# Kernel optimization log

Hardware: AMD Instinct MI355X
Metric: run time of the kernel (lower is better)

Reference implementation:

```python
import jax, jax.numpy as jnp
import numpy as np

L = 2
GRID_RES = 0.01
ATOL = 0.01
RTOL = 1e-5  # torch.isclose default rtol


def _grad_matrices(filtration, bar, sample_pts):
    # filtration: [S,2] simplex (x,y) filtration values
    # bar:        [P,R] bar length per sample point, per rank
    # sample_pts: [P,2] center points
    S = filtration.shape[0]
    P, R = bar.shape
    shift = jnp.arange(-L, L + 1, dtype=filtration.dtype)          # [5]
    fx = filtration[:, 0]
    fy = filtration[:, 1]
    ptx = sample_pts[:, 0]
    pty = sample_pts[:, 1]
    scale = bar + GRID_RES                                          # [P,R]
    line_x = shift[None, None, :] * scale[:, :, None] + ptx[:, None, None]  # [P,R,5]
    line_y = shift[None, None, :] * scale[:, :, None] + pty[:, None, None]  # [P,R,5]
    last_x = line_x[:, :, -1]                                       # [P,R]
    last_y = line_y[:, :, -1]                                       # [P,R]
    # torch.isclose(a, b, atol): |a-b| <= atol + rtol*|b|
    tol_x = ATOL + RTOL * jnp.abs(fx)                               # [S]
    tol_y = ATOL + RTOL * jnp.abs(fy)
    close_x = jnp.any(jnp.abs(line_x[:, :, None, :] - fx[None, None, :, None])
                      <= tol_x[None, None, :, None], axis=-1)       # [P,R,S]
    close_y = jnp.any(jnp.abs(line_y[:, :, None, :] - fy[None, None, :, None])
                      <= tol_y[None, None, :, None], axis=-1)       # [P,R,S]
    fsum = fx + fy                                                  # [S]
    psum = (ptx + pty)[:, None, None]                               # [P,1,1]
    below = fsum[None, None, :] < psum                              # [P,1,S]
    above = fsum[None, None, :] > psum
    cond_x = close_x & (fy[None, None, :] <= last_y[:, :, None])    # [P,R,S]
    cond_y = close_y & (fx[None, None, :] <= last_x[:, :, None])
    lower_x = cond_x & below
    upper_x = cond_x & above
    lower_y = cond_y & below
    upper_y = cond_y & above
    gx = jnp.where(upper_x, 1.0, jnp.where(lower_x, -1.0, 0.0))     # [P,R,S]
    gy = jnp.where(upper_y, 1.0, jnp.where(lower_y, -1.0, 0.0))
    # interleave x/y per simplex: columns (2s, 2s+1)
    gm = jnp.stack([gx, gy], axis=-1).reshape(P, R, 2 * S).transpose(1, 0, 2)  # [R,P,2S]
    any_s = lambda m: jnp.any(m, axis=2)                            # [P,R]
    cx = jnp.where(any_s(upper_x), -1.0, jnp.where(any_s(lower_x), 1.0, 0.0))
    cy = jnp.where(any_s(upper_y), -1.0, jnp.where(any_s(lower_y), 1.0, 0.0))
    gc = jnp.stack([cx, cy], axis=-1).transpose(1, 0, 2)            # [R,P,2]
    return gm, gc


def setup_inputs() -> dict:
    key = jax.random.key(0)
    k1, k2, k3, k4 = jax.random.split(key, 4)
    S, P, R = 2000, 2500, 5
    filtration = jax.random.uniform(k1, (S, 2), dtype=jnp.float32)
    bars_h0 = jax.random.uniform(k2, (P, R), dtype=jnp.float32)
    bars_h1 = jax.random.uniform(k3, (P, R), dtype=jnp.float32)
    sample_pts = jax.random.uniform(k4, (P, 2), dtype=jnp.float32)
    return {"filtration": filtration, "bars_h0": bars_h0,
            "bars_h1": bars_h1, "sample_pts": sample_pts}


def reference(filtration, bars_h0, bars_h1, sample_pts):
    # moveSimplices.forward: passes bars through and builds the sparse
    # per-point gradient matrices (the dominant compute) for H0 and H1.
    gm0, gc0 = _grad_matrices(filtration, bars_h0, sample_pts)
    gm1, gc1 = _grad_matrices(filtration, bars_h1, sample_pts)
    out = jnp.stack([bars_h0, bars_h1])  # forward returns (bars[0], bars[1])
    return out, gm0, gc0, gm1, gc1
```

## Files before the change

### kernel.cpp

```cpp
#include <hip/hip_runtime.h>

#define S 2000
#define P 2500
#define R 5
#define HALF (S / 2)
#define NIT 16

typedef float floatx4 __attribute__((ext_vector_type(4)));

__global__ __launch_bounds__(256) void grad_kernel(
    const float* __restrict__ filtration,
    const float* __restrict__ bars0,
    const float* __restrict__ bars1,
    const float* __restrict__ sample_pts,
    float* __restrict__ out,
    float* __restrict__ gm0, float* __restrict__ gc0,
    float* __restrict__ gm1, float* __restrict__ gc1)
{
    __shared__ floatx4 sf[HALF];

    int tid = threadIdx.x;
    const floatx4* filt4 = (const floatx4*)filtration;
#pragma unroll
    for (int i = 0; i < NIT / 4; ++i) {
        int idx = tid + 256 * i;
        if (idx < HALF) sf[idx] = filt4[idx];
    }

    int job = blockIdx.x * 4 + (tid >> 6);
    int lane = tid & 63;
    int h = job / (R * P);
    int rem = job - h * (R * P);
    int r = rem / P;
    int p = rem - r * P;

    const float* bars = h ? bars1 : bars0;
    float* gm = h ? gm1 : gm0;
    float* gc = h ? gc1 : gc0;

    float bar = bars[p * R + r];
    float scale = bar + 0.01f;
    float ptx = sample_pts[2 * p];
    float pty = sample_pts[2 * p + 1];
    float psum = ptx + pty;

    float lxk[5], lyk[5];
#pragma unroll
    for (int k = 0; k < 5; ++k) {
        float ks = (float)(k - 2) * scale;
        lxk[k] = ks + ptx;
        lyk[k] = ks + pty;
    }
    float lastx = lxk[4];
    float lasty = lyk[4];

    if (lane == 0) out[(size_t)h * (P * R) + p * R + r] = bar;

    float* gmrow = gm + ((size_t)rem) * (size_t)(2 * S);

    bool aUx = false, aLx = false, aUy = false, aLy = false;

    __syncthreads();

#pragma unroll
    for (int it = 0; it < NIT; ++it) {
        int j = lane + 64 * it;
        if (it < NIT - 1 || j < HALF) {
            floatx4 f = sf[j];
            floatx4 o;
            {
                float fx = f.x, fy = f.y;
                float tolx = __fadd_rn(0.01f, __fmul_rn(1e-5f, __builtin_fabsf(fx)));
                float toly = __fadd_rn(0.01f, __fmul_rn(1e-5f, __builtin_fabsf(fy)));
                float mx = fminf(fminf(fminf(__builtin_fabsf(lxk[0] - fx),
                                             __builtin_fabsf(lxk[1] - fx)),
                                       fminf(__builtin_fabsf(lxk[2] - fx),
                                             __builtin_fabsf(lxk[3] - fx))),
                                 __builtin_fabsf(lxk[4] - fx));
                float my = fminf(fminf(fminf(__builtin_fabsf(lyk[0] - fy),
                                             __builtin_fabsf(lyk[1] - fy)),
                                       fminf(__builtin_fabsf(lyk[2] - fy),
                                             __builtin_fabsf(lyk[3] - fy))),
                                 __builtin_fabsf(lyk[4] - fy));
                bool cx = (mx <= tolx) && (fy <= lasty);
                bool cy = (my <= toly) && (fx <= lastx);
                float fsum = fx + fy;
                bool ab = fsum > psum, be = fsum < psum;
                float sgn = ab ? 1.0f : (be ? -1.0f : 0.0f);
                o.x = cx ? sgn : 0.0f;
                o.y = cy ? sgn : 0.0f;
                aUx = aUx || (cx && ab);  aLx = aLx || (cx && be);
                aUy = aUy || (cy && ab);  aLy = aLy || (cy && be);
            }
            {
                float fx = f.z, fy = f.w;
                float tolx = __fadd_rn(0.01f, __fmul_rn(1e-5f, __builtin_fabsf(fx)));
                float toly = __fadd_rn(0.01f, __fmul_rn(1e-5f, __builtin_fabsf(fy)));
                float mx = fminf(fminf(fminf(__builtin_fabsf(lxk[0] - fx),
                                             __builtin_fabsf(lxk[1] - fx)),
                                       fminf(__builtin_fabsf(lxk[2] - fx),
                                             __builtin_fabsf(lxk[3] - fx))),
                                 __builtin_fabsf(lxk[4] - fx));
                float my = fminf(fminf(fminf(__builtin_fabsf(lyk[0] - fy),
                                             __builtin_fabsf(lyk[1] - fy)),
                                       fminf(__builtin_fabsf(lyk[2] - fy),
                                             __builtin_fabsf(lyk[3] - fy))),
                                 __builtin_fabsf(lyk[4] - fy));
                bool cx = (mx <= tolx) && (fy <= lasty);
                bool cy = (my <= toly) && (fx <= lastx);
                float fsum = fx + fy;
                bool ab = fsum > psum, be = fsum < psum;
                float sgn = ab ? 1.0f : (be ? -1.0f : 0.0f);
                o.z = cx ? sgn : 0.0f;
                o.w = cy ? sgn : 0.0f;
                aUx = aUx || (cx && ab);  aLx = aLx || (cx && be);
                aUy = aUy || (cy && ab);  aLy = aLy || (cy && be);
            }
            *(floatx4*)(gmrow + (size_t)j * 4) = o;
        }
    }

    bool anyUx = __any(aUx);
    bool anyLx = __any(aLx);
    bool anyUy = __any(aUy);
    bool anyLy = __any(aLy);
    if (lane == 0) {
        float cxv = anyUx ? -1.0f : (anyLx ? 1.0f : 0.0f);
        float cyv = anyUy ? -1.0f : (anyLy ? 1.0f : 0.0f);
        *(float2*)(gc + ((size_t)rem) * 2) = make_float2(cxv, cyv);
    }
}

extern "C" void kernel_launch(void* const* d_in, const int* in_sizes, int n_in,
                              void* d_out, int out_size, void* d_ws, size_t ws_size,
                              hipStream_t stream) {
    const float* filtration = (const float*)d_in[0];
    const float* bars_h0    = (const float*)d_in[1];
    const float* bars_h1    = (const float*)d_in[2];
    const float* sample_pts = (const float*)d_in[3];

    float* out = (float*)d_out;
    float* o_stack = out;
    float* gm0     = o_stack + (size_t)2 * P * R;
    float* gc0     = gm0 + (size_t)R * P * 2 * S;
    float* gm1     = gc0 + (size_t)R * P * 2;
    float* gc1     = gm1 + (size_t)R * P * 2 * S;

    grad_kernel<<<(2 * R * P) / 4, 256, 0, stream>>>(filtration, bars_h0, bars_h1, sample_pts,
                                                     o_stack, gm0, gc0, gm1, gc1);
}
```

Before: 84.92 us.

## Flatten gm writes into persistent grid-stride loop with atomic row flags

Replaces the one-wave-per-row kernel with a persistent grid of 768 workgroups. Each wave walks the flattened 25M float4 output in contiguous chunks that may span two rows, so the write stream stays dense and the per-row tail of 1000 float4s no longer leaves lanes idle. The per-row any-flags are reduced with shuffles and combined through atomicOr into a workspace array. A separate finalize kernel then writes gc and the bars passthrough. This adds two extra kernel launches, per-element recomputation of line parameters, and atomics, all in exchange for better store streaming and less launch and tail overhead.

```diff
diff --git a/kernel.cpp b/kernel.cpp
--- a/kernel.cpp
+++ b/kernel.cpp
@@ -4,131 +4,179 @@
 #define P 2500
 #define R 5
 #define HALF (S / 2)
-#define NIT 16
+#define ROWS_PER_H 12500
+#define TOTAL_ROWS 25000
+#define TOTAL4 25000000
+#define HTHRESH4 12500000
+#define GM0_OFF4 6250
+#define GC_GAP4 6250
+#define NWG 768
+#define NW (NWG * 4)
+#define UF 4
 
 typedef float floatx4 __attribute__((ext_vector_type(4)));
 
-__global__ __launch_bounds__(256) void grad_kernel(
+__global__ void zero_flags(unsigned* __restrict__ wsflags) {
+    int i = blockIdx.x * 256 + threadIdx.x;
+    if (i < TOTAL_ROWS) wsflags[i] = 0u;
+}
+
+__global__ __launch_bounds__(256) void grad_main(
     const float* __restrict__ filtration,
     const float* __restrict__ bars0,
     const float* __restrict__ bars1,
     const float* __restrict__ sample_pts,
-    float* __restrict__ out,
-    float* __restrict__ gm0, float* __restrict__ gc0,
-    float* __restrict__ gm1, float* __restrict__ gc1)
+    float* __restrict__ obase,
+    unsigned* __restrict__ wsflags)
 {
     __shared__ floatx4 sf[HALF];
-
     int tid = threadIdx.x;
     const floatx4* filt4 = (const floatx4*)filtration;
-#pragma unroll
-    for (int i = 0; i < NIT / 4; ++i) {
-        int idx = tid + 256 * i;
-        if (idx < HALF) sf[idx] = filt4[idx];
-    }
-
-    int job = blockIdx.x * 4 + (tid >> 6);
-    int lane = tid & 63;
-    int h = job / (R * P);
-    int rem = job - h * (R * P);
-    int r = rem / P;
-    int p = rem - r * P;
-
-    const float* bars = h ? bars1 : bars0;
-    float* gm = h ? gm1 : gm0;
-    float* gc = h ? gc1 : gc0;
-
-    float bar = bars[p * R + r];
-    float scale = bar + 0.01f;
-    float ptx = sample_pts[2 * p];
-    float pty = sample_pts[2 * p + 1];
-    float psum = ptx + pty;
-
-    float lxk[5], lyk[5];
-#pragma unroll
-    for (int k = 0; k < 5; ++k) {
-        float ks = (float)(k - 2) * scale;
-        lxk[k] = ks + ptx;
-        lyk[k] = ks + pty;
-    }
-    float lastx = lxk[4];
-    float lasty = lyk[4];
-
-    if (lane == 0) out[(size_t)h * (P * R) + p * R + r] = bar;
-
-    float* gmrow = gm + ((size_t)rem) * (size_t)(2 * S);
-
-    bool aUx = false, aLx = false, aUy = false, aLy = false;
-
+    for (int i = tid; i < HALF; i += 256) sf[i] = filt4[i];
     __syncthreads();
 
+    int wid = __builtin_amdgcn_readfirstlane(blockIdx.x * 4 + (tid >> 6));
+    int lane = tid & 63;
+    floatx4* o4 = (floatx4*)obase;
+
+#pragma unroll 1
+    for (int g0 = wid * (UF * 64); g0 < TOTAL4; g0 += NW * UF * 64) {
+        int rlo = g0 / 1000;
+        int jlo = g0 - rlo * 1000;
+        int rhi = (g0 + UF * 64 - 1) / 1000;
+
+        int hlo = rlo >= ROWS_PER_H;
+        int rrlo = rlo - (hlo ? ROWS_PER_H : 0);
+        int r_lo = rrlo / P, p_lo = rrlo - (rrlo / P) * P;
+        const float* bl = hlo ? bars1 : bars0;
+        float bar_lo = bl[p_lo * R + r_lo];
+        float ptx_lo = sample_pts[2 * p_lo];
+        float pty_lo = sample_pts[2 * p_lo + 1];
+
+        int hhi = rhi >= ROWS_PER_H;
+        int rrhi = rhi - (hhi ? ROWS_PER_H : 0);
+        int r_hi = rrhi / P, p_hi = rrhi - (rrhi / P) * P;
+        const float* bh = hhi ? bars1 : bars0;
+        float bar_hi = bh[p_hi * R + r_hi];
+        float ptx_hi = sample_pts[2 * p_hi];
+        float pty_hi = sample_pts[2 * p_hi + 1];
+
+        unsigned fl_lo = 0u, fl_hi = 0u;
+
 #pragma unroll
-    for (int it = 0; it < NIT; ++it) {
-        int j = lane + 64 * it;
-        if (it < NIT - 1 || j < HALF) {
-            floatx4 f = sf[j];
-            floatx4 o;
-            {
-                float fx = f.x, fy = f.y;
-                float tolx = __fadd_rn(0.01f, __fmul_rn(1e-5f, __builtin_fabsf(fx)));
-                float toly = __fadd_rn(0.01f, __fmul_rn(1e-5f, __builtin_fabsf(fy)));
-                float mx = fminf(fminf(fminf(__builtin_fabsf(lxk[0] - fx),
-                                             __builtin_fabsf(lxk[1] - fx)),
-                                       fminf(__builtin_fabsf(lxk[2] - fx),
-                                             __builtin_fabsf(lxk[3] - fx))),
-                                 __builtin_fabsf(lxk[4] - fx));
-                float my = fminf(fminf(fminf(__builtin_fabsf(lyk[0] - fy),
-                                             __builtin_fabsf(lyk[1] - fy)),
-                                       fminf(__builtin_fabsf(lyk[2] - fy),
-                                             __builtin_fabsf(lyk[3] - fy))),
-                                 __builtin_fabsf(lyk[4] - fy));
-                bool cx = (mx <= tolx) && (fy <= lasty);
-                bool cy = (my <= toly) && (fx <= lastx);
-                float fsum = fx + fy;
-                bool ab = fsum > psum, be = fsum < psum;
-                float sgn = ab ? 1.0f : (be ? -1.0f : 0.0f);
-                o.x = cx ? sgn : 0.0f;
-                o.y = cy ? sgn : 0.0f;
-                aUx = aUx || (cx && ab);  aLx = aLx || (cx && be);
-                aUy = aUy || (cy && ab);  aLy = aLy || (cy && be);
+        for (int c = 0; c < UF; ++c) {
+            int gcb = g0 + 64 * c;
+            if (gcb < TOTAL4) {
+                int g = gcb + lane;
+                int jj = jlo + 64 * c + lane;
+                bool hi = jj >= 1000;
+                int j = hi ? jj - 1000 : jj;
+
+                float bar = hi ? bar_hi : bar_lo;
+                float ptx = hi ? ptx_hi : ptx_lo;
+                float pty = hi ? pty_hi : pty_lo;
+                float scale = bar + 0.01f;
+                float psum = ptx + pty;
+
+                float lxk[5], lyk[5];
+#pragma unroll
+                for (int k = 0; k < 5; ++k) {
+                    float ks = (float)(k - 2) * scale;
+                    lxk[k] = ks + ptx;
+                    lyk[k] = ks + pty;
+                }
+                float lastx = lxk[4];
+                float lasty = lyk[4];
+
+                floatx4 f = sf[j];
+                floatx4 o;
+                unsigned flags = 0u;
+                {
+                    float fx = f.x, fy = f.y;
+                    float tolx = __fadd_rn(0.01f, __fmul_rn(1e-5f, __builtin_fabsf(fx)));
+                    float toly = __fadd_rn(0.01f, __fmul_rn(1e-5f, __builtin_fabsf(fy)));
+                    float mx = fminf(fminf(fminf(__builtin_fabsf(lxk[0] - fx),
+                                                 __builtin_fabsf(lxk[1] - fx)),
+                                           fminf(__builtin_fabsf(lxk[2] - fx),
+                                                 __builtin_fabsf(lxk[3] - fx))),
+                                     __builtin_fabsf(lxk[4] - fx));
+                    float my = fminf(fminf(fminf(__builtin_fabsf(lyk[0] - fy),
+                                                 __builtin_fabsf(lyk[1] - fy)),
+                                           fminf(__builtin_fabsf(lyk[2] - fy),
+                                                 __builtin_fabsf(lyk[3] - fy))),
+                                     __builtin_fabsf(lyk[4] - fy));
+                    bool cx = (mx <= tolx) && (fy <= lasty);
+                    bool cy = (my <= toly) && (fx <= lastx);
+                    float fsum = fx + fy;
+                    bool ab = fsum > psum, be = fsum < psum;
+                    float sgn = ab ? 1.0f : (be ? -1.0f : 0.0f);
+                    o.x = cx ? sgn : 0.0f;
+                    o.y = cy ? sgn : 0.0f;
+                    flags |= (cx && ab) ? 1u : 0u;  flags |= (cx && be) ? 2u : 0u;
+                    flags |= (cy && ab) ? 4u : 0u;  flags |= (cy && be) ? 8u : 0u;
+                }
+                {
+                    float fx = f.z, fy = f.w;
+                    float tolx = __fadd_rn(0.01f, __fmul_rn(1e-5f, __builtin_fabsf(fx)));
+                    float toly = __fadd_rn(0.01f, __fmul_rn(1e-5f, __builtin_fabsf(fy)));
+                    float mx = fminf(fminf(fminf(__builtin_fabsf(lxk[0] - fx),
+                                                 __builtin_fabsf(lxk[1] - fx)),
+                                           fminf(__builtin_fabsf(lxk[2] - fx),
+                                                 __builtin_fabsf(lxk[3] - fx))),
+                                     __builtin_fabsf(lxk[4] - fx));
+                    float my = fminf(fminf(fminf(__builtin_fabsf(lyk[0] - fy),
+                                                 __builtin_fabsf(lyk[1] - fy)),
+                                           fminf(__builtin_fabsf(lyk[2] - fy),
+                                                 __builtin_fabsf(lyk[3] - fy))),
+                                     __builtin_fabsf(lyk[4] - fy));
+                    bool cx = (mx <= tolx) && (fy <= lasty);
+                    bool cy = (my <= toly) && (fx <= lastx);
+                    float fsum = fx + fy;
+                    bool ab = fsum > psum, be = fsum < psum;
+                    float sgn = ab ? 1.0f : (be ? -1.0f : 0.0f);
+                    o.z = cx ? sgn : 0.0f;
+                    o.w = cy ? sgn : 0.0f;
+                    flags |= (cx && ab) ? 1u : 0u;  flags |= (cx && be) ? 2u : 0u;
+                    flags |= (cy && ab) ? 4u : 0u;  flags |= (cy && be) ? 8u : 0u;
+                }
+                fl_lo |= hi ? 0u : flags;
+                fl_hi |= hi ? flags : 0u;
+
+                int a4 = GM0_OFF4 + g + ((g >= HTHRESH4) ? GC_GAP4 : 0);
+                o4[a4] = o;
             }
-            {
-                float fx = f.z, fy = f.w;
-                float tolx = __fadd_rn(0.01f, __fmul_rn(1e-5f, __builtin_fabsf(fx)));
-                float toly = __fadd_rn(0.01f, __fmul_rn(1e-5f, __builtin_fabsf(fy)));
-                float mx = fminf(fminf(fminf(__builtin_fabsf(lxk[0] - fx),
-                                             __builtin_fabsf(lxk[1] - fx)),
-                                       fminf(__builtin_fabsf(lxk[2] - fx),
-                                             __builtin_fabsf(lxk[3] - fx))),
-                                 __builtin_fabsf(lxk[4] - fx));
-                float my = fminf(fminf(fminf(__builtin_fabsf(lyk[0] - fy),
-                                             __builtin_fabsf(lyk[1] - fy)),
-                                       fminf(__builtin_fabsf(lyk[2] - fy),
-                                             __builtin_fabsf(lyk[3] - fy))),
-                                 __builtin_fabsf(lyk[4] - fy));
-                bool cx = (mx <= tolx) && (fy <= lasty);
-                bool cy = (my <= toly) && (fx <= lastx);
-                float fsum = fx + fy;
-                bool ab = fsum > psum, be = fsum < psum;
-                float sgn = ab ? 1.0f : (be ? -1.0f : 0.0f);
-                o.z = cx ? sgn : 0.0f;
-                o.w = cy ? sgn : 0.0f;
-                aUx = aUx || (cx && ab);  aLx = aLx || (cx && be);
-                aUy = aUy || (cy && ab);  aLy = aLy || (cy && be);
-            }
-            *(floatx4*)(gmrow + (size_t)j * 4) = o;
+        }
+
+        unsigned comb = fl_lo | (fl_hi << 4);
+#pragma unroll
+        for (int m = 1; m < 64; m <<= 1)
+            comb |= (unsigned)__shfl_xor((int)comb, m);
+        if (lane == 0) {
+            unsigned lo = comb & 0xFu;
+            unsigned hi = (comb >> 4) & 0xFu;
+            if (lo) atomicOr(&wsflags[rlo], lo);
+            if (hi) atomicOr(&wsflags[rhi], hi);
         }
     }
+}
 
-    bool anyUx = __any(aUx);
-    bool anyLx = __any(aLx);
-    bool anyUy = __any(aUy);
-    bool anyLy = __any(aLy);
-    if (lane == 0) {
-        float cxv = anyUx ? -1.0f : (anyLx ? 1.0f : 0.0f);
-        float cyv = anyUy ? -1.0f : (anyLy ? 1.0f : 0.0f);
-        *(float2*)(gc + ((size_t)rem) * 2) = make_float2(cxv, cyv);
-    }
+__global__ void finalize(const float* __restrict__ bars0,
+                         const float* __restrict__ bars1,
+                         const unsigned* __restrict__ wsflags,
+                         float* __restrict__ obase)
+{
+    int i = blockIdx.x * 256 + threadIdx.x;
+    if (i >= TOTAL_ROWS) return;
+    int h = i >= ROWS_PER_H;
+    int rr = i - (h ? ROWS_PER_H : 0);
+    int r = rr / P, p = rr - r * P;
+    unsigned b = wsflags[i];
+    float cxv = (b & 1u) ? -1.0f : ((b & 2u) ? 1.0f : 0.0f);
+    float cyv = (b & 4u) ? -1.0f : ((b & 8u) ? 1.0f : 0.0f);
+    float* gc = obase + (h ? 100050000 : 50025000);
+    gc[rr * 2] = cxv;
+    gc[rr * 2 + 1] = cyv;
+    obase[h * (P * R) + p * R + r] = (h ? bars1 : bars0)[p * R + r];
 }
 
 extern "C" void kernel_launch(void* const* d_in, const int* in_sizes, int n_in,
@@ -139,13 +187,12 @@
     const float* bars_h1    = (const float*)d_in[2];
     const float* sample_pts = (const float*)d_in[3];
 
-    float* out = (float*)d_out;
-    float* o_stack = out;
-    float* gm0     = o_stack + (size_t)2 * P * R;
-    float* gc0     = gm0 + (size_t)R * P * 2 * S;
-    float* gm1     = gc0 + (size_t)R * P * 2;
-    float* gc1     = gm1 + (size_t)R * P * 2 * S;
+    float* obase = (float*)d_out;
+    unsigned* wsflags = (unsigned*)d_ws;
 
-    grad_kernel<<<(2 * R * P) / 4, 256, 0, stream>>>(filtration, bars_h0, bars_h1, sample_pts,
-                                                     o_stack, gm0, gc0, gm1, gc1);
+    zero_flags<<<(TOTAL_ROWS + 255) / 256, 256, 0, stream>>>(wsflags);
+    grad_main<<<NWG, 256, 0, stream>>>(filtration, bars_h0, bars_h1, sample_pts,
+                                       obase, wsflags);
+    finalize<<<(TOTAL_ROWS + 255) / 256, 256, 0, stream>>>(bars_h0, bars_h1,
+                                                           wsflags, obase);
 }
```

Measured after the change: 93.93 us. 10.6% more time.
